# Kernel tuning notes

Hardware: AMD Instinct MI355X
Metric: run time of the kernel (lower is better)

The kernel has to match this reference:

```python
import jax, jax.numpy as jnp
import numpy as np

N_NODES = 100000


def setup_inputs() -> dict:
    key = jax.random.key(0)
    k1, k2, k3 = jax.random.split(key, 3)
    x = jax.random.normal(k1, (N_NODES, 128), dtype=jnp.float32)
    edge_index = jax.random.randint(k2, (2, 1600000), 0, N_NODES, dtype=jnp.int64)
    # GCNConv linear weight (hidden, input) and bias; PReLU slope (init 0.25 as in torch)
    W = jax.random.normal(k3, (128, 128), dtype=jnp.float32) * (1.0 / np.sqrt(128))
    b = jnp.zeros((128,), dtype=jnp.float32)
    prelu_a = jnp.full((1,), 0.25, dtype=jnp.float32)
    return {"x": x, "edge_index": edge_index, "W": W, "b": b, "prelu_a": prelu_a}


def reference(x, edge_index, W, b, prelu_a):
    n = x.shape[0]
    # add self loops (as in forward's add_self_loops)
    loop = jnp.arange(n, dtype=edge_index.dtype)
    src = jnp.concatenate([edge_index[0], loop])  # [E+N]
    dst = jnp.concatenate([edge_index[1], loop])
    # linear transform first (small GEMM), then gather/scatter on hidden dim
    h = x @ W.T  # [N, H]
    # symmetric degree normalization 1/sqrt(deg_src * deg_dst), deg = in-degree incl. self-loop
    ones = jnp.ones_like(dst, dtype=h.dtype)
    deg = jax.ops.segment_sum(ones, dst, num_segments=n)
    dinv = jnp.where(deg > 0, jax.lax.rsqrt(deg), 0.0)  # [N]
    norm = dinv[src] * dinv[dst]  # [E+N]
    msg = h[src] * norm[:, None]  # gather + scale, memory-bound
    out = jax.ops.segment_sum(msg, dst, num_segments=n) + b  # scatter-add
    # PReLU (single shared slope); dropout is identity in eval mode
    out = jnp.where(out >= 0, out, prelu_a[0] * out)
    return out
```

## Files before the change

### kernel.cpp

```cpp
#include <hip/hip_runtime.h>
#include <math.h>

#define HDIM 128
#define BSH 9
#define CH 4096

typedef __attribute__((ext_vector_type(8))) short short8;
typedef __attribute__((ext_vector_type(4))) float f32x4;

__device__ inline unsigned short bf16_hi(float f) {
    return (unsigned short)(__float_as_uint(f) >> 16);
}
__device__ inline unsigned short bf16_rn(float f) {
    unsigned int u = __float_as_uint(f);
    return (unsigned short)((u + 0x7FFF + ((u >> 16) & 1)) >> 16);
}

__global__ __launch_bounds__(256) void binA_kernel(
    const int* __restrict__ dst, int E, int* __restrict__ bcnt) {
    __shared__ int hist[256];
    const int t = threadIdx.x;
    const int c0 = blockIdx.x * CH;
    hist[t] = 0;
    __syncthreads();
    #pragma unroll
    for (int k = 0; k < CH / 256; ++k) {
        int e = c0 + t + (k << 8);
        if (e < E) atomicAdd(&hist[dst[e] >> BSH], 1);
    }
    __syncthreads();
    if (hist[t] > 0) atomicAdd(&bcnt[t], hist[t]);
}

__global__ __launch_bounds__(256) void scanB_kernel(
    const int* __restrict__ bcnt, int* __restrict__ bbase, int* __restrict__ bcur,
    int* __restrict__ row_ptr, int NB, int n, int E) {
    __shared__ int s[256];
    const int t = threadIdx.x;
    int v = (t < NB) ? bcnt[t] : 0;
    s[t] = v;
    __syncthreads();
    for (int off = 1; off < 256; off <<= 1) {
        int u = (t >= off) ? s[t - off] : 0;
        __syncthreads();
        s[t] += u;
        __syncthreads();
    }
    int excl = s[t] - v;
    if (t < NB) { bbase[t] = excl; bcur[t] = excl; }
    if (t == 0) { bbase[NB] = E; row_ptr[n] = E; }
}

__global__ __launch_bounds__(256) void binB_kernel(
    const int* __restrict__ ei, int E,
    int* __restrict__ bcur, unsigned int* __restrict__ eb) {
    __shared__ int hist[256], base[256], cur[256];
    const int t = threadIdx.x;
    const int c0 = blockIdx.x * CH;
    hist[t] = 0;
    __syncthreads();

    int sv[CH / 256], dv[CH / 256];
    #pragma unroll
    for (int k = 0; k < CH / 256; ++k) {
        int e = c0 + t + (k << 8);
        if (e < E) {
            sv[k] = ei[e];
            dv[k] = ei[E + e];
            atomicAdd(&hist[dv[k] >> BSH], 1);
        } else {
            dv[k] = -1;
        }
    }
    __syncthreads();
    if (hist[t] > 0) base[t] = atomicAdd(&bcur[t], hist[t]);
    cur[t] = 0;
    __syncthreads();
    #pragma unroll
    for (int k = 0; k < CH / 256; ++k) {
        if (dv[k] >= 0) {
            int bkt = dv[k] >> BSH;
            int o = atomicAdd(&cur[bkt], 1);
            eb[(size_t)base[bkt] + o] =
                ((unsigned int)(dv[k] & ((1 << BSH) - 1)) << 23) | (unsigned int)sv[k];
        }
    }
}

__global__ __launch_bounds__(512) void binC_kernel(
    const unsigned int* __restrict__ eb, const int* __restrict__ bbase,
    int* __restrict__ row_ptr, float* __restrict__ dinv,
    int* __restrict__ col, int n) {
    __shared__ int hist[512];
    __shared__ int cur[512];
    const int t = threadIdx.x;
    const int b = blockIdx.x;
    const int node0 = b << BSH;
    const int e0 = bbase[b];
    const int e1 = bbase[b + 1];

    hist[t] = 0;
    __syncthreads();
    for (int e = e0 + t; e < e1; e += 512)
        atomicAdd(&hist[eb[e] >> 23], 1);
    __syncthreads();
    int v = hist[t];
    for (int off = 1; off < 512; off <<= 1) {
        int u = (t >= off) ? hist[t - off] : 0;
        __syncthreads();
        hist[t] += u;
        __syncthreads();
    }
    int excl = hist[t] - v;
    int node = node0 + t;
    if (node < n) {
        row_ptr[node] = e0 + excl;
        dinv[node] = rsqrtf((float)v + 1.0f);
    }
    cur[t] = e0 + excl;
    __syncthreads();
    for (int e = e0 + t; e < e1; e += 512) {
        unsigned int p = eb[e];
        int pos = atomicAdd(&cur[p >> 23], 1);
        col[pos] = (int)(p & 0x7FFFFF);
    }
}

__global__ __launch_bounds__(256) void mfma_gemm_kernel(
    const float* __restrict__ x, const float* __restrict__ W,
    const float* __restrict__ dinv, unsigned short* __restrict__ gb, int n) {
    __shared__ uint4 Wh[2048];
    __shared__ uint4 Wl[2048];

    const int t = threadIdx.x;
    const int wave = t >> 6;
    const int lane = t & 63;
    const int q = lane >> 4;
    const int m = lane & 15;

    for (int idx = t; idx < 2048; idx += 256) {
        const int j = idx >> 4;
        const int c = idx & 15;
        const float4* wp = (const float4*)(W + (size_t)j * HDIM + c * 8);
        float4 va = wp[0], vb = wp[1];
        float vs[8] = {va.x, va.y, va.z, va.w, vb.x, vb.y, vb.z, vb.w};
        unsigned short h[8], l[8];
        #pragma unroll
        for (int k = 0; k < 8; ++k) {
            h[k] = bf16_hi(vs[k]);
            float hf = __uint_as_float((unsigned int)h[k] << 16);
            l[k] = bf16_hi(vs[k] - hf);
        }
        uint4 hch, lch;
        hch.x = (unsigned int)h[0] | ((unsigned int)h[1] << 16);
        hch.y = (unsigned int)h[2] | ((unsigned int)h[3] << 16);
        hch.z = (unsigned int)h[4] | ((unsigned int)h[5] << 16);
        hch.w = (unsigned int)h[6] | ((unsigned int)h[7] << 16);
        lch.x = (unsigned int)l[0] | ((unsigned int)l[1] << 16);
        lch.y = (unsigned int)l[2] | ((unsigned int)l[3] << 16);
        lch.z = (unsigned int)l[4] | ((unsigned int)l[5] << 16);
        lch.w = (unsigned int)l[6] | ((unsigned int)l[7] << 16);
        const int sidx = (j << 4) | (c ^ (j & 15));
        Wh[sidx] = hch;
        Wl[sidx] = lch;
    }
    __syncthreads();

    const int ngroups = (n + 127) >> 7;
    for (int grp = blockIdx.x; grp < ngroups; grp += gridDim.x) {
        const int rowbase = (grp << 7) + (wave << 5);

        f32x4 acc[2][8];
        #pragma unroll
        for (int mt = 0; mt < 2; ++mt)
            #pragma unroll
            for (int ct = 0; ct < 8; ++ct)
                acc[mt][ct] = (f32x4){0.f, 0.f, 0.f, 0.f};

        #pragma unroll
        for (int kk = 0; kk < 4; ++kk) {
            short8 ah[2], al[2];
            #pragma unroll
            for (int mt = 0; mt < 2; ++mt) {
                const int r = rowbase + (mt << 4) + m;
                float vs[8];
                if (r < n) {
                    const float4* xp = (const float4*)(x + (size_t)r * HDIM + (kk << 5) + (q << 3));
                    float4 va = xp[0], vb = xp[1];
                    vs[0] = va.x; vs[1] = va.y; vs[2] = va.z; vs[3] = va.w;
                    vs[4] = vb.x; vs[5] = vb.y; vs[6] = vb.z; vs[7] = vb.w;
                } else {
                    #pragma unroll
                    for (int k = 0; k < 8; ++k) vs[k] = 0.f;
                }
                #pragma unroll
                for (int k = 0; k < 8; ++k) {
                    unsigned short h = bf16_hi(vs[k]);
                    float hf = __uint_as_float((unsigned int)h << 16);
                    unsigned short lo = bf16_hi(vs[k] - hf);
                    ah[mt][k] = (short)h;
                    al[mt][k] = (short)lo;
                }
            }
            #pragma unroll
            for (int ct = 0; ct < 8; ++ct) {
                const int nn = (ct << 4) + m;
                const int sidx = (nn << 4) | (((kk << 2) + q) ^ m);
                short8 bh = *(const short8*)&Wh[sidx];
                short8 bl = *(const short8*)&Wl[sidx];
                #pragma unroll
                for (int mt = 0; mt < 2; ++mt) {
                    acc[mt][ct] = __builtin_amdgcn_mfma_f32_16x16x32_bf16(ah[mt], bh, acc[mt][ct], 0, 0, 0);
                    acc[mt][ct] = __builtin_amdgcn_mfma_f32_16x16x32_bf16(al[mt], bh, acc[mt][ct], 0, 0, 0);
                    acc[mt][ct] = __builtin_amdgcn_mfma_f32_16x16x32_bf16(ah[mt], bl, acc[mt][ct], 0, 0, 0);
                }
            }
        }

        #pragma unroll
        for (int mt = 0; mt < 2; ++mt) {
            #pragma unroll
            for (int rr = 0; rr < 4; ++rr) {
                const int grow = rowbase + (mt << 4) + (q << 2) + rr;
                if (grow < n) {
                    const float di = dinv[grow];
                    unsigned short* gp = gb + (size_t)grow * HDIM + m;
                    #pragma unroll
                    for (int ct = 0; ct < 8; ++ct)
                        gp[ct << 4] = bf16_rn(acc[mt][ct][rr] * di);
                }
            }
        }
    }
}

__global__ __launch_bounds__(256) void gather_kernel(
    const int* __restrict__ row_ptr, const int* __restrict__ col,
    const uint4* __restrict__ gbr, const float* __restrict__ dinv,
    const float* __restrict__ bias, const float* __restrict__ prelu_a,
    float* __restrict__ out, int n) {
    const int wv = threadIdx.x >> 6;
    const int lane = threadIdx.x & 63;
    const int q = lane >> 4;
    const int l16 = lane & 15;
    const int i = blockIdx.x * 4 + wv;
    if (i >= n) return;

    const int beg = row_ptr[i];
    const int end = row_ptr[i + 1];

    float a[8];
    #pragma unroll
    for (int k = 0; k < 8; ++k) a[k] = 0.f;

    if (q == 0) {
        uint4 u = gbr[(size_t)i * 16 + l16];
        a[0] += __uint_as_float(u.x << 16);
        a[1] += __uint_as_float(u.x & 0xffff0000u);
        a[2] += __uint_as_float(u.y << 16);
        a[3] += __uint_as_float(u.y & 0xffff0000u);
        a[4] += __uint_as_float(u.z << 16);
        a[5] += __uint_as_float(u.z & 0xffff0000u);
        a[6] += __uint_as_float(u.w << 16);
        a[7] += __uint_as_float(u.w & 0xffff0000u);
    }

    int e = beg + q;
    for (; e + 4 < end; e += 8) {
        int s0 = col[e];
        int s1 = col[e + 4];
        uint4 u0 = gbr[(size_t)s0 * 16 + l16];
        uint4 u1 = gbr[(size_t)s1 * 16 + l16];
        a[0] += __uint_as_float(u0.x << 16);       a[0] += __uint_as_float(u1.x << 16);
        a[1] += __uint_as_float(u0.x & 0xffff0000u); a[1] += __uint_as_float(u1.x & 0xffff0000u);
        a[2] += __uint_as_float(u0.y << 16);       a[2] += __uint_as_float(u1.y << 16);
        a[3] += __uint_as_float(u0.y & 0xffff0000u); a[3] += __uint_as_float(u1.y & 0xffff0000u);
        a[4] += __uint_as_float(u0.z << 16);       a[4] += __uint_as_float(u1.z << 16);
        a[5] += __uint_as_float(u0.z & 0xffff0000u); a[5] += __uint_as_float(u1.z & 0xffff0000u);
        a[6] += __uint_as_float(u0.w << 16);       a[6] += __uint_as_float(u1.w << 16);
        a[7] += __uint_as_float(u0.w & 0xffff0000u); a[7] += __uint_as_float(u1.w & 0xffff0000u);
    }
    if (e < end) {
        int s = col[e];
        uint4 u = gbr[(size_t)s * 16 + l16];
        a[0] += __uint_as_float(u.x << 16);
        a[1] += __uint_as_float(u.x & 0xffff0000u);
        a[2] += __uint_as_float(u.y << 16);
        a[3] += __uint_as_float(u.y & 0xffff0000u);
        a[4] += __uint_as_float(u.z << 16);
        a[5] += __uint_as_float(u.z & 0xffff0000u);
        a[6] += __uint_as_float(u.w << 16);
        a[7] += __uint_as_float(u.w & 0xffff0000u);
    }

    #pragma unroll
    for (int k = 0; k < 8; ++k) {
        a[k] += __shfl_xor(a[k], 16);
        a[k] += __shfl_xor(a[k], 32);
    }

    const float di = dinv[i];
    const float aa = prelu_a[0];
    const int c0 = (l16 << 3) + (q << 1);
    float2 bb = *(const float2*)(bias + c0);
    float v0 = di * a[(q << 1) + 0] + bb.x;
    float v1 = di * a[(q << 1) + 1] + bb.y;
    v0 = v0 >= 0.f ? v0 : aa * v0;
    v1 = v1 >= 0.f ? v1 : aa * v1;
    *(float2*)(out + (size_t)i * HDIM + c0) = make_float2(v0, v1);
}

extern "C" void kernel_launch(void* const* d_in, const int* in_sizes, int n_in,
                              void* d_out, int out_size, void* d_ws, size_t ws_size,
                              hipStream_t stream) {
    const float* x  = (const float*)d_in[0];
    const int*   ei = (const int*)d_in[1];
    const float* W  = (const float*)d_in[2];
    const float* b  = (const float*)d_in[3];
    const float* pa = (const float*)d_in[4];

    const int n = in_sizes[0] / HDIM;
    const int E = in_sizes[1] / 2;
    const int NB = (n + (1 << BSH) - 1) >> BSH;

    float* out = (float*)d_out;

    unsigned short* gb      = (unsigned short*)d_ws;
    unsigned int*   eb      = (unsigned int*)(gb + (size_t)n * HDIM);
    float*          dinv    = (float*)(eb + (size_t)E);
    int*            row_ptr = (int*)(dinv + n);
    int*            col     = row_ptr + (n + 1);
    int*            bcnt    = col + E;
    int*            bbase   = bcnt + 256;
    int*            bcur    = bbase + 257;

    hipMemsetAsync(bcnt, 0, 256 * sizeof(int), stream);

    const int nchunk = (E + CH - 1) / CH;
    binA_kernel<<<nchunk, 256, 0, stream>>>(ei + E, E, bcnt);
    scanB_kernel<<<1, 256, 0, stream>>>(bcnt, bbase, bcur, row_ptr, NB, n, E);
    binB_kernel<<<nchunk, 256, 0, stream>>>(ei, E, bcur, eb);
    binC_kernel<<<NB, 512, 0, stream>>>(eb, bbase, row_ptr, dinv, col, n);
    mfma_gemm_kernel<<<512, 256, 0, stream>>>(x, W, dinv, gb, n);
    gather_kernel<<<(n + 3) / 4, 256, 0, stream>>>(row_ptr, col, (const uint4*)gb, dinv, b, pa, out, n);
}
```

Before: 260.9 us.

## Fuse bucket scan into binA, stage-sort binB writes in LDS, wave-scan binC

The separate single-block scan kernel is removed: the last binA block, detected with a global done counter, performs the bucket prefix scan, which saves one launch. binB now sorts each chunk's edges by bucket in shared memory and writes them out contiguously per bucket, replacing scattered atomic-offset stores with coalesced runs. binC replaces its 512-wide barrier-based scan with wavefront shuffle scans. The costs are more LDS in binB, which may lower occupancy, and a last-block fence pattern that relies on correct memory ordering.

Result: slower. 270.8 us (+3.8%).

```diff
diff --git a/kernel.cpp b/kernel.cpp
--- a/kernel.cpp
+++ b/kernel.cpp
@@ -17,8 +17,11 @@
 }
 
 __global__ __launch_bounds__(256) void binA_kernel(
-    const int* __restrict__ dst, int E, int* __restrict__ bcnt) {
+    const int* __restrict__ dst, int E, int* __restrict__ bcnt,
+    int* __restrict__ done, int* __restrict__ bbase, int* __restrict__ bcur,
+    int* __restrict__ row_ptr, int NB, int n, int nblocks) {
     __shared__ int hist[256];
+    __shared__ int lastflag;
     const int t = threadIdx.x;
     const int c0 = blockIdx.x * CH;
     hist[t] = 0;
@@ -30,23 +33,23 @@
     }
     __syncthreads();
     if (hist[t] > 0) atomicAdd(&bcnt[t], hist[t]);
-}
-
-__global__ __launch_bounds__(256) void scanB_kernel(
-    const int* __restrict__ bcnt, int* __restrict__ bbase, int* __restrict__ bcur,
-    int* __restrict__ row_ptr, int NB, int n, int E) {
-    __shared__ int s[256];
-    const int t = threadIdx.x;
-    int v = (t < NB) ? bcnt[t] : 0;
-    s[t] = v;
+    __threadfence();
+    if (t == 0) {
+        int old = atomicAdd(done, 1);
+        lastflag = (old == nblocks - 1) ? 1 : 0;
+    }
+    __syncthreads();
+    if (!lastflag) return;
+    int v = (t < NB) ? atomicAdd(&bcnt[t], 0) : 0;
+    hist[t] = v;
     __syncthreads();
     for (int off = 1; off < 256; off <<= 1) {
-        int u = (t >= off) ? s[t - off] : 0;
+        int u = (t >= off) ? hist[t - off] : 0;
         __syncthreads();
-        s[t] += u;
+        hist[t] += u;
         __syncthreads();
     }
-    int excl = s[t] - v;
+    int excl = hist[t] - v;
     if (t < NB) { bbase[t] = excl; bcur[t] = excl; }
     if (t == 0) { bbase[NB] = E; row_ptr[n] = E; }
 }
@@ -54,36 +57,55 @@
 __global__ __launch_bounds__(256) void binB_kernel(
     const int* __restrict__ ei, int E,
     int* __restrict__ bcur, unsigned int* __restrict__ eb) {
-    __shared__ int hist[256], base[256], cur[256];
+    __shared__ int hist[256];
+    __shared__ int lbase[256];
+    __shared__ int gbase[256];
+    __shared__ unsigned int sorted[CH];
+    __shared__ unsigned char sbkt[CH];
     const int t = threadIdx.x;
     const int c0 = blockIdx.x * CH;
+    const int CHn = min(CH, E - c0);
     hist[t] = 0;
     __syncthreads();
 
-    int sv[CH / 256], dv[CH / 256];
+    unsigned int pk[CH / 256];
+    int bk[CH / 256], rk[CH / 256];
     #pragma unroll
     for (int k = 0; k < CH / 256; ++k) {
         int e = c0 + t + (k << 8);
         if (e < E) {
-            sv[k] = ei[e];
-            dv[k] = ei[E + e];
-            atomicAdd(&hist[dv[k] >> BSH], 1);
+            int s = ei[e];
+            int d = ei[E + e];
+            pk[k] = ((unsigned int)(d & ((1 << BSH) - 1)) << 23) | (unsigned int)s;
+            bk[k] = d >> BSH;
+            rk[k] = atomicAdd(&hist[bk[k]], 1);
         } else {
-            dv[k] = -1;
-        }
-    }
-    __syncthreads();
-    if (hist[t] > 0) base[t] = atomicAdd(&bcur[t], hist[t]);
-    cur[t] = 0;
+            bk[k] = -1;
+        }
+    }
+    __syncthreads();
+    int v = hist[t];
+    for (int off = 1; off < 256; off <<= 1) {
+        int u = (t >= off) ? hist[t - off] : 0;
+        __syncthreads();
+        hist[t] += u;
+        __syncthreads();
+    }
+    lbase[t] = hist[t] - v;
+    if (v > 0) gbase[t] = atomicAdd(&bcur[t], v);
     __syncthreads();
     #pragma unroll
     for (int k = 0; k < CH / 256; ++k) {
-        if (dv[k] >= 0) {
-            int bkt = dv[k] >> BSH;
-            int o = atomicAdd(&cur[bkt], 1);
-            eb[(size_t)base[bkt] + o] =
-                ((unsigned int)(dv[k] & ((1 << BSH) - 1)) << 23) | (unsigned int)sv[k];
-        }
+        if (bk[k] >= 0) {
+            int p = lbase[bk[k]] + rk[k];
+            sorted[p] = pk[k];
+            sbkt[p] = (unsigned char)bk[k];
+        }
+    }
+    __syncthreads();
+    for (int idx = t; idx < CHn; idx += 256) {
+        int b = sbkt[idx];
+        eb[(size_t)gbase[b] + (idx - lbase[b])] = sorted[idx];
     }
 }
 
@@ -93,6 +115,7 @@
     int* __restrict__ col, int n) {
     __shared__ int hist[512];
     __shared__ int cur[512];
+    __shared__ int wsum[8];
     const int t = threadIdx.x;
     const int b = blockIdx.x;
     const int node0 = b << BSH;
@@ -104,14 +127,27 @@
     for (int e = e0 + t; e < e1; e += 512)
         atomicAdd(&hist[eb[e] >> 23], 1);
     __syncthreads();
-    int v = hist[t];
-    for (int off = 1; off < 512; off <<= 1) {
-        int u = (t >= off) ? hist[t - off] : 0;
-        __syncthreads();
-        hist[t] += u;
-        __syncthreads();
-    }
-    int excl = hist[t] - v;
+    const int v = hist[t];
+    int x = v;
+    #pragma unroll
+    for (int off = 1; off < 64; off <<= 1) {
+        int u = __shfl_up(x, off);
+        if ((t & 63) >= off) x += u;
+    }
+    if ((t & 63) == 63) wsum[t >> 6] = x;
+    __syncthreads();
+    if (t < 8) {
+        int y = wsum[t];
+        #pragma unroll
+        for (int off = 1; off < 8; off <<= 1) {
+            int u = __shfl_up(y, off);
+            if (t >= off) y += u;
+        }
+        wsum[t] = y;
+    }
+    __syncthreads();
+    int excl = x - v + ((t >> 6) ? wsum[(t >> 6) - 1] : 0);
+
     int node = node0 + t;
     if (node < n) {
         row_ptr[node] = e0 + excl;
@@ -271,13 +307,13 @@
         int s1 = col[e + 4];
         uint4 u0 = gbr[(size_t)s0 * 16 + l16];
         uint4 u1 = gbr[(size_t)s1 * 16 + l16];
-        a[0] += __uint_as_float(u0.x << 16);       a[0] += __uint_as_float(u1.x << 16);
+        a[0] += __uint_as_float(u0.x << 16);         a[0] += __uint_as_float(u1.x << 16);
         a[1] += __uint_as_float(u0.x & 0xffff0000u); a[1] += __uint_as_float(u1.x & 0xffff0000u);
-        a[2] += __uint_as_float(u0.y << 16);       a[2] += __uint_as_float(u1.y << 16);
+        a[2] += __uint_as_float(u0.y << 16);         a[2] += __uint_as_float(u1.y << 16);
         a[3] += __uint_as_float(u0.y & 0xffff0000u); a[3] += __uint_as_float(u1.y & 0xffff0000u);
-        a[4] += __uint_as_float(u0.z << 16);       a[4] += __uint_as_float(u1.z << 16);
+        a[4] += __uint_as_float(u0.z << 16);         a[4] += __uint_as_float(u1.z << 16);
         a[5] += __uint_as_float(u0.z & 0xffff0000u); a[5] += __uint_as_float(u1.z & 0xffff0000u);
-        a[6] += __uint_as_float(u0.w << 16);       a[6] += __uint_as_float(u1.w << 16);
+        a[6] += __uint_as_float(u0.w << 16);         a[6] += __uint_as_float(u1.w << 16);
         a[7] += __uint_as_float(u0.w & 0xffff0000u); a[7] += __uint_as_float(u1.w & 0xffff0000u);
     }
     if (e < end) {
@@ -331,14 +367,15 @@
     int*            row_ptr = (int*)(dinv + n);
     int*            col     = row_ptr + (n + 1);
     int*            bcnt    = col + E;
-    int*            bbase   = bcnt + 256;
+    int*            done    = bcnt + 256;
+    int*            bbase   = done + 1;
     int*            bcur    = bbase + 257;
 
-    hipMemsetAsync(bcnt, 0, 256 * sizeof(int), stream);
+    hipMemsetAsync(bcnt, 0, 257 * sizeof(int), stream);
 
     const int nchunk = (E + CH - 1) / CH;
-    binA_kernel<<<nchunk, 256, 0, stream>>>(ei + E, E, bcnt);
-    scanB_kernel<<<1, 256, 0, stream>>>(bcnt, bbase, bcur, row_ptr, NB, n, E);
+    binA_kernel<<<nchunk, 256, 0, stream>>>(ei + E, E, bcnt, done, bbase, bcur,
+                                            row_ptr, NB, n, nchunk);
     binB_kernel<<<nchunk, 256, 0, stream>>>(ei, E, bcur, eb);
     binC_kernel<<<NB, 512, 0, stream>>>(eb, bbase, row_ptr, dinv, col, n);
     mfma_gemm_kernel<<<512, 256, 0, stream>>>(x, W, dinv, gb, n);
```

## Overlap GEMM with CSR binning kernels and move dinv scaling to gather

Applied to the files above, without the earlier changes.

Removes the GEMM's dependence on dinv by applying the source-side dinv scale inside the gather, which reads dinv[src] per edge. The GEMM can then be split across the binB and binC launches and run on extra blocks alongside them. The separate scan kernel is folded into binA through a last-block-done counter, and binC is moved to 256 threads with a wave-shuffle scan. Together these cut kernel launches and idle GPU time between stages. In exchange each gathered edge costs an extra dinv load, the fused kernels reserve 64KB of shared memory per block, and values are rounded to bf16 before scaling, which slightly changes numerics.

Result: slower. 274.2 us (+5.1%).

```diff
diff --git a/kernel.cpp b/kernel.cpp
--- a/kernel.cpp
+++ b/kernel.cpp
@@ -4,6 +4,8 @@
 #define HDIM 128
 #define BSH 9
 #define CH 4096
+#define GEMM_BLKS 256
+#define GSPLIT 352
 
 typedef __attribute__((ext_vector_type(8))) short short8;
 typedef __attribute__((ext_vector_type(4))) float f32x4;
@@ -17,8 +19,11 @@
 }
 
 __global__ __launch_bounds__(256) void binA_kernel(
-    const int* __restrict__ dst, int E, int* __restrict__ bcnt) {
+    const int* __restrict__ dst, int E, int* __restrict__ bcnt,
+    int* __restrict__ done, int* __restrict__ bbase, int* __restrict__ bcur,
+    int* __restrict__ row_ptr, int NB, int n, int nblocks) {
     __shared__ int hist[256];
+    __shared__ int lastflag;
     const int t = threadIdx.x;
     const int c0 = blockIdx.x * CH;
     hist[t] = 0;
@@ -30,107 +35,33 @@
     }
     __syncthreads();
     if (hist[t] > 0) atomicAdd(&bcnt[t], hist[t]);
-}
-
-__global__ __launch_bounds__(256) void scanB_kernel(
-    const int* __restrict__ bcnt, int* __restrict__ bbase, int* __restrict__ bcur,
-    int* __restrict__ row_ptr, int NB, int n, int E) {
-    __shared__ int s[256];
-    const int t = threadIdx.x;
-    int v = (t < NB) ? bcnt[t] : 0;
-    s[t] = v;
+    __threadfence();
+    if (t == 0) {
+        int old = atomicAdd(done, 1);
+        lastflag = (old == nblocks - 1) ? 1 : 0;
+    }
+    __syncthreads();
+    if (!lastflag) return;
+    int v = (t < NB) ? atomicAdd(&bcnt[t], 0) : 0;
+    hist[t] = v;
     __syncthreads();
     for (int off = 1; off < 256; off <<= 1) {
-        int u = (t >= off) ? s[t - off] : 0;
-        __syncthreads();
-        s[t] += u;
-        __syncthreads();
-    }
-    int excl = s[t] - v;
-    if (t < NB) { bbase[t] = excl; bcur[t] = excl; }
-    if (t == 0) { bbase[NB] = E; row_ptr[n] = E; }
-}
-
-__global__ __launch_bounds__(256) void binB_kernel(
-    const int* __restrict__ ei, int E,
-    int* __restrict__ bcur, unsigned int* __restrict__ eb) {
-    __shared__ int hist[256], base[256], cur[256];
-    const int t = threadIdx.x;
-    const int c0 = blockIdx.x * CH;
-    hist[t] = 0;
-    __syncthreads();
-
-    int sv[CH / 256], dv[CH / 256];
-    #pragma unroll
-    for (int k = 0; k < CH / 256; ++k) {
-        int e = c0 + t + (k << 8);
-        if (e < E) {
-            sv[k] = ei[e];
-            dv[k] = ei[E + e];
-            atomicAdd(&hist[dv[k] >> BSH], 1);
-        } else {
-            dv[k] = -1;
-        }
-    }
-    __syncthreads();
-    if (hist[t] > 0) base[t] = atomicAdd(&bcur[t], hist[t]);
-    cur[t] = 0;
-    __syncthreads();
-    #pragma unroll
-    for (int k = 0; k < CH / 256; ++k) {
-        if (dv[k] >= 0) {
-            int bkt = dv[k] >> BSH;
-            int o = atomicAdd(&cur[bkt], 1);
-            eb[(size_t)base[bkt] + o] =
-                ((unsigned int)(dv[k] & ((1 << BSH) - 1)) << 23) | (unsigned int)sv[k];
-        }
-    }
-}
-
-__global__ __launch_bounds__(512) void binC_kernel(
-    const unsigned int* __restrict__ eb, const int* __restrict__ bbase,
-    int* __restrict__ row_ptr, float* __restrict__ dinv,
-    int* __restrict__ col, int n) {
-    __shared__ int hist[512];
-    __shared__ int cur[512];
-    const int t = threadIdx.x;
-    const int b = blockIdx.x;
-    const int node0 = b << BSH;
-    const int e0 = bbase[b];
-    const int e1 = bbase[b + 1];
-
-    hist[t] = 0;
-    __syncthreads();
-    for (int e = e0 + t; e < e1; e += 512)
-        atomicAdd(&hist[eb[e] >> 23], 1);
-    __syncthreads();
-    int v = hist[t];
-    for (int off = 1; off < 512; off <<= 1) {
         int u = (t >= off) ? hist[t - off] : 0;
         __syncthreads();
         hist[t] += u;
         __syncthreads();
     }
     int excl = hist[t] - v;
-    int node = node0 + t;
-    if (node < n) {
-        row_ptr[node] = e0 + excl;
-        dinv[node] = rsqrtf((float)v + 1.0f);
-    }
-    cur[t] = e0 + excl;
-    __syncthreads();
-    for (int e = e0 + t; e < e1; e += 512) {
-        unsigned int p = eb[e];
-        int pos = atomicAdd(&cur[p >> 23], 1);
-        col[pos] = (int)(p & 0x7FFFFF);
-    }
-}
-
-__global__ __launch_bounds__(256) void mfma_gemm_kernel(
+    if (t < NB) { bbase[t] = excl; bcur[t] = excl; }
+    if (t == 0) { bbase[NB] = E; row_ptr[n] = E; }
+}
+
+__device__ __forceinline__ void gemm_body(
     const float* __restrict__ x, const float* __restrict__ W,
-    const float* __restrict__ dinv, unsigned short* __restrict__ gb, int n) {
-    __shared__ uint4 Wh[2048];
-    __shared__ uint4 Wl[2048];
+    unsigned short* __restrict__ gb, int n,
+    int g0, int g1, int bid, int nblk, char* smem_raw) {
+    uint4* Wh = (uint4*)smem_raw;
+    uint4* Wl = ((uint4*)smem_raw) + 2048;
 
     const int t = threadIdx.x;
     const int wave = t >> 6;
@@ -166,8 +97,7 @@
     }
     __syncthreads();
 
-    const int ngroups = (n + 127) >> 7;
-    for (int grp = blockIdx.x; grp < ngroups; grp += gridDim.x) {
+    for (int grp = g0 + bid; grp < g1; grp += nblk) {
         const int rowbase = (grp << 7) + (wave << 5);
 
         f32x4 acc[2][8];
@@ -223,15 +153,132 @@
             for (int rr = 0; rr < 4; ++rr) {
                 const int grow = rowbase + (mt << 4) + (q << 2) + rr;
                 if (grow < n) {
-                    const float di = dinv[grow];
                     unsigned short* gp = gb + (size_t)grow * HDIM + m;
                     #pragma unroll
                     for (int ct = 0; ct < 8; ++ct)
-                        gp[ct << 4] = bf16_rn(acc[mt][ct][rr] * di);
+                        gp[ct << 4] = bf16_rn(acc[mt][ct][rr]);
                 }
             }
         }
     }
+}
+
+__device__ __forceinline__ void binB_body(
+    const int* __restrict__ ei, int E,
+    int* __restrict__ bcur, unsigned int* __restrict__ eb,
+    int chunk, char* smem_raw) {
+    int* hist = (int*)smem_raw;
+    int* base = hist + 256;
+    int* cur  = base + 256;
+    const int t = threadIdx.x;
+    const int c0 = chunk * CH;
+    hist[t] = 0;
+    __syncthreads();
+
+    int sv[CH / 256], dv[CH / 256];
+    #pragma unroll
+    for (int k = 0; k < CH / 256; ++k) {
+        int e = c0 + t + (k << 8);
+        if (e < E) {
+            sv[k] = ei[e];
+            dv[k] = ei[E + e];
+            atomicAdd(&hist[dv[k] >> BSH], 1);
+        } else {
+            dv[k] = -1;
+        }
+    }
+    __syncthreads();
+    if (hist[t] > 0) base[t] = atomicAdd(&bcur[t], hist[t]);
+    cur[t] = 0;
+    __syncthreads();
+    #pragma unroll
+    for (int k = 0; k < CH / 256; ++k) {
+        if (dv[k] >= 0) {
+            int bkt = dv[k] >> BSH;
+            int o = atomicAdd(&cur[bkt], 1);
+            eb[(size_t)base[bkt] + o] =
+                ((unsigned int)(dv[k] & ((1 << BSH) - 1)) << 23) | (unsigned int)sv[k];
+        }
+    }
+}
+
+__device__ __forceinline__ void binC_body(
+    const unsigned int* __restrict__ eb, const int* __restrict__ bbase,
+    int* __restrict__ row_ptr, float* __restrict__ dinv,
+    int* __restrict__ col, int n, int b, char* smem_raw) {
+    int* hist = (int*)smem_raw;
+    int* cur  = hist + 512;
+    int* wsum = cur + 512;
+    const int t = threadIdx.x;
+    const int node0 = b << BSH;
+    const int e0 = bbase[b];
+    const int e1 = bbase[b + 1];
+
+    hist[t] = 0; hist[t + 256] = 0;
+    __syncthreads();
+    for (int e = e0 + t; e < e1; e += 256)
+        atomicAdd(&hist[eb[e] >> 23], 1);
+    __syncthreads();
+    const int v0 = hist[2 * t];
+    const int v1 = hist[2 * t + 1];
+    const int pt = v0 + v1;
+    int xp = pt;
+    #pragma unroll
+    for (int off = 1; off < 64; off <<= 1) {
+        int u = __shfl_up(xp, off);
+        if ((t & 63) >= off) xp += u;
+    }
+    if ((t & 63) == 63) wsum[t >> 6] = xp;
+    __syncthreads();
+    if (t < 4) {
+        int y = wsum[t];
+        #pragma unroll
+        for (int off = 1; off < 4; off <<= 1) {
+            int u = __shfl_up(y, off);
+            if (t >= off) y += u;
+        }
+        wsum[t] = y;
+    }
+    __syncthreads();
+    const int px = xp - pt + ((t >> 6) ? wsum[(t >> 6) - 1] : 0);
+    const int c0 = e0 + px, c1 = e0 + px + v0;
+    cur[2 * t] = c0;
+    cur[2 * t + 1] = c1;
+    int node = node0 + 2 * t;
+    if (node < n)     { row_ptr[node] = c0;     dinv[node] = rsqrtf((float)v0 + 1.0f); }
+    if (node + 1 < n) { row_ptr[node + 1] = c1; dinv[node + 1] = rsqrtf((float)v1 + 1.0f); }
+    __syncthreads();
+    for (int e = e0 + t; e < e1; e += 256) {
+        unsigned int p = eb[e];
+        int pos = atomicAdd(&cur[p >> 23], 1);
+        col[pos] = (int)(p & 0x7FFFFF);
+    }
+}
+
+__global__ __launch_bounds__(256) void fuseB_kernel(
+    const int* __restrict__ ei, int E, int* __restrict__ bcur,
+    unsigned int* __restrict__ eb,
+    const float* __restrict__ x, const float* __restrict__ W,
+    unsigned short* __restrict__ gb, int n, int nchunk) {
+    __shared__ __attribute__((aligned(16))) char smem[65536];
+    const int bid = blockIdx.x;
+    if (bid < nchunk)
+        binB_body(ei, E, bcur, eb, bid, smem);
+    else
+        gemm_body(x, W, gb, n, 0, GSPLIT, bid - nchunk, GEMM_BLKS, smem);
+}
+
+__global__ __launch_bounds__(256) void fuseC_kernel(
+    const unsigned int* __restrict__ eb, const int* __restrict__ bbase,
+    int* __restrict__ row_ptr, float* __restrict__ dinv, int* __restrict__ col,
+    const float* __restrict__ x, const float* __restrict__ W,
+    unsigned short* __restrict__ gb, int n, int NB, int ngroups) {
+    __shared__ __attribute__((aligned(16))) char smem[65536];
+    const int bid = blockIdx.x;
+    if (bid < NB)
+        binC_body(eb, bbase, row_ptr, dinv, col, n, bid, smem);
+    else
+        gemm_body(x, W, gb, n, GSPLIT, ngroups, bid - NB, GEMM_BLKS, smem);
 }
 
 __global__ __launch_bounds__(256) void gather_kernel(
@@ -248,6 +295,7 @@
 
     const int beg = row_ptr[i];
     const int end = row_ptr[i + 1];
+    const float di = dinv[i];
 
     float a[8];
     #pragma unroll
@@ -255,42 +303,53 @@
 
     if (q == 0) {
         uint4 u = gbr[(size_t)i * 16 + l16];
-        a[0] += __uint_as_float(u.x << 16);
-        a[1] += __uint_as_float(u.x & 0xffff0000u);
-        a[2] += __uint_as_float(u.y << 16);
-        a[3] += __uint_as_float(u.y & 0xffff0000u);
-        a[4] += __uint_as_float(u.z << 16);
-        a[5] += __uint_as_float(u.z & 0xffff0000u);
-        a[6] += __uint_as_float(u.w << 16);
-        a[7] += __uint_as_float(u.w & 0xffff0000u);
+        a[0] = fmaf(di, __uint_as_float(u.x << 16), a[0]);
+        a[1] = fmaf(di, __uint_as_float(u.x & 0xffff0000u), a[1]);
+        a[2] = fmaf(di, __uint_as_float(u.y << 16), a[2]);
+        a[3] = fmaf(di, __uint_as_float(u.y & 0xffff0000u), a[3]);
+        a[4] = fmaf(di, __uint_as_float(u.z << 16), a[4]);
+        a[5] = fmaf(di, __uint_as_float(u.z & 0xffff0000u), a[5]);
+        a[6] = fmaf(di, __uint_as_float(u.w << 16), a[6]);
+        a[7] = fmaf(di, __uint_as_float(u.w & 0xffff0000u), a[7]);
     }
 
     int e = beg + q;
     for (; e + 4 < end; e += 8) {
         int s0 = col[e];
         int s1 = col[e + 4];
+        float d0 = dinv[s0];
+        float d1 = dinv[s1];
         uint4 u0 = gbr[(size_t)s0 * 16 + l16];
         uint4 u1 = gbr[(size_t)s1 * 16 + l16];
-        a[0] += __uint_as_float(u0.x << 16);       a[0] += __uint_as_float(u1.x << 16);
-        a[1] += __uint_as_float(u0.x & 0xffff0000u); a[1] += __uint_as_float(u1.x & 0xffff0000u);
-        a[2] += __uint_as_float(u0.y << 16);       a[2] += __uint_as_float(u1.y << 16);
-        a[3] += __uint_as_float(u0.y & 0xffff0000u); a[3] += __uint_as_float(u1.y & 0xffff0000u);
-        a[4] += __uint_as_float(u0.z << 16);       a[4] += __uint_as_float(u1.z << 16);
-        a[5] += __uint_as_float(u0.z & 0xffff0000u); a[5] += __uint_as_float(u1.z & 0xffff0000u);
-        a[6] += __uint_as_float(u0.w << 16);       a[6] += __uint_as_float(u1.w << 16);
-        a[7] += __uint_as_float(u0.w & 0xffff0000u); a[7] += __uint_as_float(u1.w & 0xffff0000u);
+        a[0] = fmaf(d0, __uint_as_float(u0.x << 16), a[0]);
+        a[1] = fmaf(d0, __uint_as_float(u0.x & 0xffff0000u), a[1]);
+        a[2] = fmaf(d0, __uint_as_float(u0.y << 16), a[2]);
+        a[3] = fmaf(d0, __uint_as_float(u0.y & 0xffff0000u), a[3]);
+        a[4] = fmaf(d0, __uint_as_float(u0.z << 16), a[4]);
+        a[5] = fmaf(d0, __uint_as_float(u0.z & 0xffff0000u), a[5]);
+        a[6] = fmaf(d0, __uint_as_float(u0.w << 16), a[6]);
+        a[7] = fmaf(d0, __uint_as_float(u0.w & 0xffff0000u), a[7]);
+        a[0] = fmaf(d1, __uint_as_float(u1.x << 16), a[0]);
+        a[1] = fmaf(d1, __uint_as_float(u1.x & 0xffff0000u), a[1]);
+        a[2] = fmaf(d1, __uint_as_float(u1.y << 16), a[2]);
+        a[3] = fmaf(d1, __uint_as_float(u1.y & 0xffff0000u), a[3]);
+        a[4] = fmaf(d1, __uint_as_float(u1.z << 16), a[4]);
+        a[5] = fmaf(d1, __uint_as_float(u1.z & 0xffff0000u), a[5]);
+        a[6] = fmaf(d1, __uint_as_float(u1.w << 16), a[6]);
+        a[7] = fmaf(d1, __uint_as_float(u1.w & 0xffff0000u), a[7]);
     }
     if (e < end) {
         int s = col[e];
+        float d = dinv[s];
         uint4 u = gbr[(size_t)s * 16 + l16];
-        a[0] += __uint_as_float(u.x << 16);
-        a[1] += __uint_as_float(u.x & 0xffff0000u);
-        a[2] += __uint_as_float(u.y << 16);
-        a[3] += __uint_as_float(u.y & 0xffff0000u);
-        a[4] += __uint_as_float(u.z << 16);
-        a[5] += __uint_as_float(u.z & 0xffff0000u);
-        a[6] += __uint_as_float(u.w << 16);
-        a[7] += __uint_as_float(u.w & 0xffff0000u);
+        a[0] = fmaf(d, __uint_as_float(u.x << 16), a[0]);
+        a[1] = fmaf(d, __uint_as_float(u.x & 0xffff0000u), a[1]);
+        a[2] = fmaf(d, __uint_as_float(u.y << 16), a[2]);
+        a[3] = fmaf(d, __uint_as_float(u.y & 0xffff0000u), a[3]);
+        a[4] = fmaf(d, __uint_as_float(u.z << 16), a[4]);
+        a[5] = fmaf(d, __uint_as_float(u.z & 0xffff0000u), a[5]);
+        a[6] = fmaf(d, __uint_as_float(u.w << 16), a[6]);
+        a[7] = fmaf(d, __uint_as_float(u.w & 0xffff0000u), a[7]);
     }
 
     #pragma unroll
@@ -299,7 +358,6 @@
         a[k] += __shfl_xor(a[k], 32);
     }
 
-    const float di = dinv[i];
     const float aa = prelu_a[0];
     const int c0 = (l16 << 3) + (q << 1);
     float2 bb = *(const float2*)(bias + c0);
@@ -322,6 +380,7 @@
     const int n = in_sizes[0] / HDIM;
     const int E = in_sizes[1] / 2;
     const int NB = (n + (1 << BSH) - 1) >> BSH;
+    const int ngroups = (n + 127) >> 7;
 
     float* out = (float*)d_out;
 
@@ -331,16 +390,18 @@
     int*            row_ptr = (int*)(dinv + n);
     int*            col     = row_ptr + (n + 1);
     int*            bcnt    = col + E;
-    int*            bbase   = bcnt + 256;
+    int*            done    = bcnt + 256;
+    int*            bbase   = done + 1;
     int*            bcur    = bbase + 257;
 
-    hipMemsetAsync(bcnt, 0, 256 * sizeof(int), stream);
+    hipMemsetAsync(bcnt, 0, 257 * sizeof(int), stream);
 
     const int nchunk = (E + CH - 1) / CH;
-    binA_kernel<<<nchunk, 256, 0, stream>>>(ei + E, E, bcnt);
-    scanB_kernel<<<1, 256, 0, stream>>>(bcnt, bbase, bcur, row_ptr, NB, n, E);
-    binB_kernel<<<nchunk, 256, 0, stream>>>(ei, E, bcur, eb);
-    binC_kernel<<<NB, 512, 0, stream>>>(eb, bbase, row_ptr, dinv, col, n);
-    mfma_gemm_kernel<<<512, 256, 0, stream>>>(x, W, dinv, gb, n);
-    gather_kernel<<<(n + 3) / 4, 256, 0, stream>>>(row_ptr, col, (const uint4*)gb, dinv, b, pa, out, n);
-}
+    binA_kernel<<<nchunk, 256, 0, stream>>>(ei + E, E, bcnt, done, bbase, bcur,
+                                            row_ptr, NB, n, nchunk);
+    fuseB_kernel<<<nchunk + GEMM_BLKS, 256, 0, stream>>>(ei, E, bcur, eb, x, W, gb, n, nchunk);
+    fuseC_kernel<<<NB + GEMM_BLKS, 256, 0, stream>>>(eb, bbase, row_ptr, dinv, col,
+                                                     x, W, gb, n, NB, ngroups);
+    gather_kernel<<<(n + 3) / 4, 256, 0, stream>>>(row_ptr, col, (const uint4*)gb,
+                                                   dinv, b, pa, out, n);
+}
```

## Overlap GEMM with edge binning by co-launching blocks, move dinv scaling to gather

Applied to the files above, without the earlier changes.

The GEMM no longer depends on dinv, so it is split into two halves that share a launch with the binA and binB histogram passes through block-index dispatch. This lets compute-heavy and atomic-heavy work run at the same time. W is pre-split into bf16 hi/lo halves once by a small prep kernel and then read from global memory instead of swizzled LDS. To make this possible, the source-side dinv scaling moves into the gather as a per-edge fmaf, which adds extra dinv loads per edge. The gather is unrolled to four edges per step, and the binC scan uses wave shuffles.

Result: faster. 255.5 us (-2.1%).

```diff
diff --git a/kernel.cpp b/kernel.cpp
--- a/kernel.cpp
+++ b/kernel.cpp
@@ -4,6 +4,8 @@
 #define HDIM 128
 #define BSH 9
 #define CH 4096
+#define GEMM_BLKS 256
+#define GSPLIT 160
 
 typedef __attribute__((ext_vector_type(8))) short short8;
 typedef __attribute__((ext_vector_type(4))) float f32x4;
@@ -16,128 +18,9 @@
     return (unsigned short)((u + 0x7FFF + ((u >> 16) & 1)) >> 16);
 }
 
-__global__ __launch_bounds__(256) void binA_kernel(
-    const int* __restrict__ dst, int E, int* __restrict__ bcnt) {
-    __shared__ int hist[256];
-    const int t = threadIdx.x;
-    const int c0 = blockIdx.x * CH;
-    hist[t] = 0;
-    __syncthreads();
-    #pragma unroll
-    for (int k = 0; k < CH / 256; ++k) {
-        int e = c0 + t + (k << 8);
-        if (e < E) atomicAdd(&hist[dst[e] >> BSH], 1);
-    }
-    __syncthreads();
-    if (hist[t] > 0) atomicAdd(&bcnt[t], hist[t]);
-}
-
-__global__ __launch_bounds__(256) void scanB_kernel(
-    const int* __restrict__ bcnt, int* __restrict__ bbase, int* __restrict__ bcur,
-    int* __restrict__ row_ptr, int NB, int n, int E) {
-    __shared__ int s[256];
-    const int t = threadIdx.x;
-    int v = (t < NB) ? bcnt[t] : 0;
-    s[t] = v;
-    __syncthreads();
-    for (int off = 1; off < 256; off <<= 1) {
-        int u = (t >= off) ? s[t - off] : 0;
-        __syncthreads();
-        s[t] += u;
-        __syncthreads();
-    }
-    int excl = s[t] - v;
-    if (t < NB) { bbase[t] = excl; bcur[t] = excl; }
-    if (t == 0) { bbase[NB] = E; row_ptr[n] = E; }
-}
-
-__global__ __launch_bounds__(256) void binB_kernel(
-    const int* __restrict__ ei, int E,
-    int* __restrict__ bcur, unsigned int* __restrict__ eb) {
-    __shared__ int hist[256], base[256], cur[256];
-    const int t = threadIdx.x;
-    const int c0 = blockIdx.x * CH;
-    hist[t] = 0;
-    __syncthreads();
-
-    int sv[CH / 256], dv[CH / 256];
-    #pragma unroll
-    for (int k = 0; k < CH / 256; ++k) {
-        int e = c0 + t + (k << 8);
-        if (e < E) {
-            sv[k] = ei[e];
-            dv[k] = ei[E + e];
-            atomicAdd(&hist[dv[k] >> BSH], 1);
-        } else {
-            dv[k] = -1;
-        }
-    }
-    __syncthreads();
-    if (hist[t] > 0) base[t] = atomicAdd(&bcur[t], hist[t]);
-    cur[t] = 0;
-    __syncthreads();
-    #pragma unroll
-    for (int k = 0; k < CH / 256; ++k) {
-        if (dv[k] >= 0) {
-            int bkt = dv[k] >> BSH;
-            int o = atomicAdd(&cur[bkt], 1);
-            eb[(size_t)base[bkt] + o] =
-                ((unsigned int)(dv[k] & ((1 << BSH) - 1)) << 23) | (unsigned int)sv[k];
-        }
-    }
-}
-
-__global__ __launch_bounds__(512) void binC_kernel(
-    const unsigned int* __restrict__ eb, const int* __restrict__ bbase,
-    int* __restrict__ row_ptr, float* __restrict__ dinv,
-    int* __restrict__ col, int n) {
-    __shared__ int hist[512];
-    __shared__ int cur[512];
-    const int t = threadIdx.x;
-    const int b = blockIdx.x;
-    const int node0 = b << BSH;
-    const int e0 = bbase[b];
-    const int e1 = bbase[b + 1];
-
-    hist[t] = 0;
-    __syncthreads();
-    for (int e = e0 + t; e < e1; e += 512)
-        atomicAdd(&hist[eb[e] >> 23], 1);
-    __syncthreads();
-    int v = hist[t];
-    for (int off = 1; off < 512; off <<= 1) {
-        int u = (t >= off) ? hist[t - off] : 0;
-        __syncthreads();
-        hist[t] += u;
-        __syncthreads();
-    }
-    int excl = hist[t] - v;
-    int node = node0 + t;
-    if (node < n) {
-        row_ptr[node] = e0 + excl;
-        dinv[node] = rsqrtf((float)v + 1.0f);
-    }
-    cur[t] = e0 + excl;
-    __syncthreads();
-    for (int e = e0 + t; e < e1; e += 512) {
-        unsigned int p = eb[e];
-        int pos = atomicAdd(&cur[p >> 23], 1);
-        col[pos] = (int)(p & 0x7FFFFF);
-    }
-}
-
-__global__ __launch_bounds__(256) void mfma_gemm_kernel(
-    const float* __restrict__ x, const float* __restrict__ W,
-    const float* __restrict__ dinv, unsigned short* __restrict__ gb, int n) {
-    __shared__ uint4 Wh[2048];
-    __shared__ uint4 Wl[2048];
-
-    const int t = threadIdx.x;
-    const int wave = t >> 6;
-    const int lane = t & 63;
-    const int q = lane >> 4;
-    const int m = lane & 15;
-
+__global__ __launch_bounds__(256) void prep_kernel(
+    const float* __restrict__ W, uint4* __restrict__ Whg, uint4* __restrict__ Wlg) {
+    const int t = threadIdx.x;
     for (int idx = t; idx < 2048; idx += 256) {
         const int j = idx >> 4;
         const int c = idx & 15;
@@ -160,14 +43,22 @@
         lch.y = (unsigned int)l[2] | ((unsigned int)l[3] << 16);
         lch.z = (unsigned int)l[4] | ((unsigned int)l[5] << 16);
         lch.w = (unsigned int)l[6] | ((unsigned int)l[7] << 16);
-        const int sidx = (j << 4) | (c ^ (j & 15));
-        Wh[sidx] = hch;
-        Wl[sidx] = lch;
-    }
-    __syncthreads();
-
-    const int ngroups = (n + 127) >> 7;
-    for (int grp = blockIdx.x; grp < ngroups; grp += gridDim.x) {
+        Whg[idx] = hch;
+        Wlg[idx] = lch;
+    }
+}
+
+__device__ __forceinline__ void gemm_body(
+    const float* __restrict__ x, const uint4* __restrict__ Whg,
+    const uint4* __restrict__ Wlg, unsigned short* __restrict__ gb, int n,
+    int g0, int g1, int bid, int nblk) {
+    const int t = threadIdx.x;
+    const int wave = t >> 6;
+    const int lane = t & 63;
+    const int q = lane >> 4;
+    const int m = lane & 15;
+
+    for (int grp = g0 + bid; grp < g1; grp += nblk) {
         const int rowbase = (grp << 7) + (wave << 5);
 
         f32x4 acc[2][8];
@@ -205,9 +96,9 @@
             #pragma unroll
             for (int ct = 0; ct < 8; ++ct) {
                 const int nn = (ct << 4) + m;
-                const int sidx = (nn << 4) | (((kk << 2) + q) ^ m);
-                short8 bh = *(const short8*)&Wh[sidx];
-                short8 bl = *(const short8*)&Wl[sidx];
+                const int fidx = (nn << 4) | ((kk << 2) + q);
+                short8 bh = *(const short8*)&Whg[fidx];
+                short8 bl = *(const short8*)&Wlg[fidx];
                 #pragma unroll
                 for (int mt = 0; mt < 2; ++mt) {
                     acc[mt][ct] = __builtin_amdgcn_mfma_f32_16x16x32_bf16(ah[mt], bh, acc[mt][ct], 0, 0, 0);
@@ -223,16 +114,177 @@
             for (int rr = 0; rr < 4; ++rr) {
                 const int grow = rowbase + (mt << 4) + (q << 2) + rr;
                 if (grow < n) {
-                    const float di = dinv[grow];
                     unsigned short* gp = gb + (size_t)grow * HDIM + m;
                     #pragma unroll
                     for (int ct = 0; ct < 8; ++ct)
-                        gp[ct << 4] = bf16_rn(acc[mt][ct][rr] * di);
+                        gp[ct << 4] = bf16_rn(acc[mt][ct][rr]);
                 }
             }
         }
     }
 }
+
+__device__ __forceinline__ void binA_body(
+    const int* __restrict__ dst, int E, int* __restrict__ bcnt,
+    int chunk, int* hist) {
+    const int t = threadIdx.x;
+    const int c0 = chunk * CH;
+    hist[t] = 0;
+    __syncthreads();
+    #pragma unroll
+    for (int k = 0; k < CH / 256; ++k) {
+        int e = c0 + t + (k << 8);
+        if (e < E) atomicAdd(&hist[dst[e] >> BSH], 1);
+    }
+    __syncthreads();
+    if (hist[t] > 0) atomicAdd(&bcnt[t], hist[t]);
+}
+
+__device__ __forceinline__ void binB_body(
+    const int* __restrict__ ei, int E,
+    int* __restrict__ bcur, unsigned int* __restrict__ eb,
+    int chunk, int* hist, int* base, int* cur) {
+    const int t = threadIdx.x;
+    const int c0 = chunk * CH;
+    hist[t] = 0;
+    __syncthreads();
+
+    int sv[CH / 256], dv[CH / 256];
+    #pragma unroll
+    for (int k = 0; k < CH / 256; ++k) {
+        int e = c0 + t + (k << 8);
+        if (e < E) {
+            sv[k] = ei[e];
+            dv[k] = ei[E + e];
+            atomicAdd(&hist[dv[k] >> BSH], 1);
+        } else {
+            dv[k] = -1;
+        }
+    }
+    __syncthreads();
+    if (hist[t] > 0) base[t] = atomicAdd(&bcur[t], hist[t]);
+    cur[t] = 0;
+    __syncthreads();
+    #pragma unroll
+    for (int k = 0; k < CH / 256; ++k) {
+        if (dv[k] >= 0) {
+            int bkt = dv[k] >> BSH;
+            int o = atomicAdd(&cur[bkt], 1);
+            eb[(size_t)base[bkt] + o] =
+                ((unsigned int)(dv[k] & ((1 << BSH) - 1)) << 23) | (unsigned int)sv[k];
+        }
+    }
+}
+
+__global__ __launch_bounds__(256) void fuse1_kernel(
+    const int* __restrict__ dst, int E, int* __restrict__ bcnt,
+    const float* __restrict__ x, const uint4* __restrict__ Whg,
+    const uint4* __restrict__ Wlg, unsigned short* __restrict__ gb,
+    int n, int nchunk) {
+    __shared__ int s_a[256];
+    const int bid = blockIdx.x;
+    if (bid < GEMM_BLKS)
+        gemm_body(x, Whg, Wlg, gb, n, 0, GSPLIT, bid, GEMM_BLKS);
+    else
+        binA_body(dst, E, bcnt, bid - GEMM_BLKS, s_a);
+}
+
+__global__ __launch_bounds__(256) void scanB_kernel(
+    const int* __restrict__ bcnt, int* __restrict__ bbase, int* __restrict__ bcur,
+    int NB, int E) {
+    __shared__ int s[256];
+    const int t = threadIdx.x;
+    int v = (t < NB) ? bcnt[t] : 0;
+    s[t] = v;
+    __syncthreads();
+    for (int off = 1; off < 256; off <<= 1) {
+        int u = (t >= off) ? s[t - off] : 0;
+        __syncthreads();
+        s[t] += u;
+        __syncthreads();
+    }
+    int excl = s[t] - v;
+    if (t < NB) { bbase[t] = excl; bcur[t] = excl; }
+    if (t == 0) bbase[NB] = E;
+}
+
+__global__ __launch_bounds__(256) void fuse2_kernel(
+    const int* __restrict__ ei, int E, int* __restrict__ bcur,
+    unsigned int* __restrict__ eb,
+    const float* __restrict__ x, const uint4* __restrict__ Whg,
+    const uint4* __restrict__ Wlg, unsigned short* __restrict__ gb,
+    int n, int nchunk, int ngroups) {
+    __shared__ int s_a[256], s_b[256], s_c[256];
+    const int bid = blockIdx.x;
+    if (bid < GEMM_BLKS)
+        gemm_body(x, Whg, Wlg, gb, n, GSPLIT, ngroups, bid, GEMM_BLKS);
+    else
+        binB_body(ei, E, bcur, eb, bid - GEMM_BLKS, s_a, s_b, s_c);
+}
+
+__global__ __launch_bounds__(512) void binC_kernel(
+    const unsigned int* __restrict__ eb, const int* __restrict__ bbase,
+    int* __restrict__ row_ptr, float* __restrict__ dinv,
+    int* __restrict__ col, int n) {
+    __shared__ int hist[512];
+    __shared__ int cur[512];
+    __shared__ int wsum[8];
+    const int t = threadIdx.x;
+    const int b = blockIdx.x;
+    const int node0 = b << BSH;
+    const int e0 = bbase[b];
+    const int e1 = bbase[b + 1];
+
+    hist[t] = 0;
+    __syncthreads();
+    for (int e = e0 + t; e < e1; e += 512)
+        atomicAdd(&hist[eb[e] >> 23], 1);
+    __syncthreads();
+    const int v = hist[t];
+    int x = v;
+    #pragma unroll
+    for (int off = 1; off < 64; off <<= 1) {
+        int u = __shfl_up(x, off);
+        if ((t & 63) >= off) x += u;
+    }
+    if ((t & 63) == 63) wsum[t >> 6] = x;
+    __syncthreads();
+    if (t < 8) {
+        int y = wsum[t];
+        #pragma unroll
+        for (int off = 1; off < 8; off <<= 1) {
+            int u = __shfl_up(y, off);
+            if (t >= off) y += u;
+        }
+        wsum[t] = y;
+    }
+    __syncthreads();
+    int excl = x - v + ((t >> 6) ? wsum[(t >> 6) - 1] : 0);
+
+    int node = node0 + t;
+    if (node < n) {
+        row_ptr[node] = e0 + excl;
+        dinv[node] = rsqrtf((float)v + 1.0f);
+        if (node == n - 1) row_ptr[n] = e0 + excl + v;
+    }
+    cur[t] = e0 + excl;
+    __syncthreads();
+    for (int e = e0 + t; e < e1; e += 512) {
+        unsigned int p = eb[e];
+        int pos = atomicAdd(&cur[p >> 23], 1);
+        col[pos] = (int)(p & 0x7FFFFF);
+    }
+}
+
+#define EDGE_ACC(d, u) \
+    a[0] = fmaf(d, __uint_as_float((u).x << 16), a[0]); \
+    a[1] = fmaf(d, __uint_as_float((u).x & 0xffff0000u), a[1]); \
+    a[2] = fmaf(d, __uint_as_float((u).y << 16), a[2]); \
+    a[3] = fmaf(d, __uint_as_float((u).y & 0xffff0000u), a[3]); \
+    a[4] = fmaf(d, __uint_as_float((u).z << 16), a[4]); \
+    a[5] = fmaf(d, __uint_as_float((u).z & 0xffff0000u), a[5]); \
+    a[6] = fmaf(d, __uint_as_float((u).w << 16), a[6]); \
+    a[7] = fmaf(d, __uint_as_float((u).w & 0xffff0000u), a[7]);
 
 __global__ __launch_bounds__(256) void gather_kernel(
     const int* __restrict__ row_ptr, const int* __restrict__ col,
@@ -248,6 +300,7 @@
 
     const int beg = row_ptr[i];
     const int end = row_ptr[i + 1];
+    const float di = dinv[i];
 
     float a[8];
     #pragma unroll
@@ -255,42 +308,39 @@
 
     if (q == 0) {
         uint4 u = gbr[(size_t)i * 16 + l16];
-        a[0] += __uint_as_float(u.x << 16);
-        a[1] += __uint_as_float(u.x & 0xffff0000u);
-        a[2] += __uint_as_float(u.y << 16);
-        a[3] += __uint_as_float(u.y & 0xffff0000u);
-        a[4] += __uint_as_float(u.z << 16);
-        a[5] += __uint_as_float(u.z & 0xffff0000u);
-        a[6] += __uint_as_float(u.w << 16);
-        a[7] += __uint_as_float(u.w & 0xffff0000u);
+        EDGE_ACC(di, u)
     }
 
     int e = beg + q;
+    for (; e + 12 < end; e += 16) {
+        int s0 = col[e];
+        int s1 = col[e + 4];
+        int s2 = col[e + 8];
+        int s3 = col[e + 12];
+        float d0 = dinv[s0], d1 = dinv[s1], d2 = dinv[s2], d3 = dinv[s3];
+        uint4 u0 = gbr[(size_t)s0 * 16 + l16];
+        uint4 u1 = gbr[(size_t)s1 * 16 + l16];
+        uint4 u2 = gbr[(size_t)s2 * 16 + l16];
+        uint4 u3 = gbr[(size_t)s3 * 16 + l16];
+        EDGE_ACC(d0, u0)
+        EDGE_ACC(d1, u1)
+        EDGE_ACC(d2, u2)
+        EDGE_ACC(d3, u3)
+    }
     for (; e + 4 < end; e += 8) {
         int s0 = col[e];
         int s1 = col[e + 4];
+        float d0 = dinv[s0], d1 = dinv[s1];
         uint4 u0 = gbr[(size_t)s0 * 16 + l16];
         uint4 u1 = gbr[(size_t)s1 * 16 + l16];
-        a[0] += __uint_as_float(u0.x << 16);       a[0] += __uint_as_float(u1.x << 16);
-        a[1] += __uint_as_float(u0.x & 0xffff0000u); a[1] += __uint_as_float(u1.x & 0xffff0000u);
-        a[2] += __uint_as_float(u0.y << 16);       a[2] += __uint_as_float(u1.y << 16);
-        a[3] += __uint_as_float(u0.y & 0xffff0000u); a[3] += __uint_as_float(u1.y & 0xffff0000u);
-        a[4] += __uint_as_float(u0.z << 16);       a[4] += __uint_as_float(u1.z << 16);
-        a[5] += __uint_as_float(u0.z & 0xffff0000u); a[5] += __uint_as_float(u1.z & 0xffff0000u);
-        a[6] += __uint_as_float(u0.w << 16);       a[6] += __uint_as_float(u1.w << 16);
-        a[7] += __uint_as_float(u0.w & 0xffff0000u); a[7] += __uint_as_float(u1.w & 0xffff0000u);
+        EDGE_ACC(d0, u0)
+        EDGE_ACC(d1, u1)
     }
     if (e < end) {
         int s = col[e];
+        float d = dinv[s];
         uint4 u = gbr[(size_t)s * 16 + l16];
-        a[0] += __uint_as_float(u.x << 16);
-        a[1] += __uint_as_float(u.x & 0xffff0000u);
-        a[2] += __uint_as_float(u.y << 16);
-        a[3] += __uint_as_float(u.y & 0xffff0000u);
-        a[4] += __uint_as_float(u.z << 16);
-        a[5] += __uint_as_float(u.z & 0xffff0000u);
-        a[6] += __uint_as_float(u.w << 16);
-        a[7] += __uint_as_float(u.w & 0xffff0000u);
+        EDGE_ACC(d, u)
     }
 
     #pragma unroll
@@ -299,7 +349,6 @@
         a[k] += __shfl_xor(a[k], 32);
     }
 
-    const float di = dinv[i];
     const float aa = prelu_a[0];
     const int c0 = (l16 << 3) + (q << 1);
     float2 bb = *(const float2*)(bias + c0);
@@ -322,12 +371,15 @@
     const int n = in_sizes[0] / HDIM;
     const int E = in_sizes[1] / 2;
     const int NB = (n + (1 << BSH) - 1) >> BSH;
+    const int ngroups = (n + 127) >> 7;
 
     float* out = (float*)d_out;
 
     unsigned short* gb      = (unsigned short*)d_ws;
     unsigned int*   eb      = (unsigned int*)(gb + (size_t)n * HDIM);
-    float*          dinv    = (float*)(eb + (size_t)E);
+    uint4*          Whg     = (uint4*)(eb + (size_t)E);
+    uint4*          Wlg     = Whg + 2048;
+    float*          dinv    = (float*)(Wlg + 2048);
     int*            row_ptr = (int*)(dinv + n);
     int*            col     = row_ptr + (n + 1);
     int*            bcnt    = col + E;
@@ -337,10 +389,10 @@
     hipMemsetAsync(bcnt, 0, 256 * sizeof(int), stream);
 
     const int nchunk = (E + CH - 1) / CH;
-    binA_kernel<<<nchunk, 256, 0, stream>>>(ei + E, E, bcnt);
-    scanB_kernel<<<1, 256, 0, stream>>>(bcnt, bbase, bcur, row_ptr, NB, n, E);
-    binB_kernel<<<nchunk, 256, 0, stream>>>(ei, E, bcur, eb);
+    prep_kernel<<<1, 256, 0, stream>>>(W, Whg, Wlg);
+    fuse1_kernel<<<GEMM_BLKS + nchunk, 256, 0, stream>>>(ei + E, E, bcnt, x, Whg, Wlg, gb, n, nchunk);
+    scanB_kernel<<<1, 256, 0, stream>>>(bcnt, bbase, bcur, NB, E);
+    fuse2_kernel<<<GEMM_BLKS + nchunk, 256, 0, stream>>>(ei, E, bcur, eb, x, Whg, Wlg, gb, n, nchunk, ngroups);
     binC_kernel<<<NB, 512, 0, stream>>>(eb, bbase, row_ptr, dinv, col, n);
-    mfma_gemm_kernel<<<512, 256, 0, stream>>>(x, W, dinv, gb, n);
     gather_kernel<<<(n + 3) / 4, 256, 0, stream>>>(row_ptr, col, (const uint4*)gb, dinv, b, pa, out, n);
 }
```
